# Kernel tuning notes

Hardware: AMD Instinct MI355X
Metric: run time of the kernel (lower is better)

## Reference

```python
import jax, jax.numpy as jnp
import numpy as np

N, L, D, H = 2, 2048, 1024, 16
DK = D // H  # 64


def setup_inputs() -> dict:
    key = jax.random.key(0)
    ks = jax.random.split(key, 8)
    Xq = jax.random.normal(ks[0], (N, L, D), dtype=jnp.float32)
    Xk = jax.random.normal(ks[1], (N, L, D), dtype=jnp.float32)
    Xv = jax.random.normal(ks[2], (N, L, D), dtype=jnp.float32)
    mask_2d = jax.random.randint(ks[3], (N, L, L), 0, 2, dtype=jnp.int32)
    scale = 0.02
    Wq = jax.random.normal(ks[4], (D, D), dtype=jnp.float32) * scale
    Wk = jax.random.normal(ks[5], (D, D), dtype=jnp.float32) * scale
    Wv = jax.random.normal(ks[6], (D, D), dtype=jnp.float32) * scale
    Wo = jax.random.normal(ks[7], (D, D), dtype=jnp.float32) * scale
    return {"Xq": Xq, "Xk": Xk, "Xv": Xv, "Wq": Wq, "Wk": Wk, "Wv": Wv, "Wo": Wo, "mask_2d": mask_2d}


def reference(Xq, Xk, Xv, Wq, Wk, Wv, Wo, mask_2d):
    # Projections (bias=False). Per-head slicing in the original == reshape to [N,L,H,DK].
    Q = (Xq @ Wq).reshape(N, L, H, DK)
    K = (Xk @ Wk).reshape(N, L, H, DK)
    V = (Xv @ Wv).reshape(N, L, H, DK)
    # Scaled dot-product scores: [N, H, L, L]
    scores = jnp.einsum("blhd,bmhd->bhlm", Q, K) / jnp.sqrt(jnp.asarray(DK, scores_dtype(Q)))
    # NOTE: original uses masked_fill(mask==0, 0) BEFORE softmax (zero-fill, not -inf).
    scores = jnp.where(mask_2d[:, None, :, :] == 0, jnp.zeros((), scores.dtype), scores)
    A = jax.nn.softmax(scores, axis=-1)
    O = jnp.einsum("bhlm,bmhd->blhd", A, V).reshape(N, L, D)
    return O @ Wo


def scores_dtype(Q):
    return Q.dtype
```

## Files before the change

kernel.cpp:

```cpp
#include <hip/hip_runtime.h>
#include <hip/hip_bf16.h>

#define NB 2
#define L_SEQ 2048
#define NH 16
#define DKH 64
#define DMODEL 1024
#define MROWS (NB * L_SEQ)
#define QSCALE 0.18033688f
#define DD (DMODEL * DMODEL)

typedef __attribute__((ext_vector_type(8))) short short8;
typedef __attribute__((ext_vector_type(4))) float f32x4;
typedef __attribute__((ext_vector_type(2))) int int2v;
typedef __attribute__((ext_vector_type(4))) int int4v;

static __device__ __forceinline__ unsigned short f2bf(float f) {
    unsigned u = __float_as_uint(f);
    u += 0x7fffu + ((u >> 16) & 1u);
    return (unsigned short)(u >> 16);
}

static __device__ __forceinline__ float fexp2(float x) {
#if __has_builtin(__builtin_amdgcn_exp2f)
    return __builtin_amdgcn_exp2f(x);
#else
    return __expf(x * 0.6931471806f);
#endif
}

static __device__ __forceinline__ unsigned pk_bf16(float a, float b) {
    __hip_bfloat162 h = __float22bfloat162_rn(make_float2(a, b));
    return *reinterpret_cast<unsigned*>(&h);
}

static __device__ __forceinline__ void gll16(const void* g, void* l) {
    __builtin_amdgcn_global_load_lds(
        (const __attribute__((address_space(1))) void*)g,
        (__attribute__((address_space(3))) void*)l, 16, 0, 0);
}

static __device__ __forceinline__ int2v pl32swap(int a, int b) {
#if __has_builtin(__builtin_amdgcn_permlane32_swap)
    return __builtin_amdgcn_permlane32_swap(a, b, false, false);
#else
    const int pa = __shfl_xor(a, 32);
    const int pb = __shfl_xor(b, 32);
    const bool lo = ((threadIdx.x & 63) < 32);
    int2v r;
    r.x = lo ? a : pb;
    r.y = lo ? pa : b;
    return r;
#endif
}

static __device__ __forceinline__ int2v pl16swap(int a, int b) {
#if __has_builtin(__builtin_amdgcn_permlane16_swap)
    return __builtin_amdgcn_permlane16_swap(a, b, false, false);
#else
    const int pa = __shfl_xor(a, 16);
    const int pb = __shfl_xor(b, 16);
    const bool ev = (((threadIdx.x >> 4) & 1) == 0);
    int2v r;
    r.x = ev ? a : pb;
    r.y = ev ? pa : b;
    return r;
#endif
}

static __device__ __forceinline__ int sbfe1(int word, int off) {
#if __has_builtin(__builtin_amdgcn_sbfe)
    return __builtin_amdgcn_sbfe(word, off, 1);
#else
    return (word << (31 - off)) >> 31;
#endif
}

__global__ __launch_bounds__(256)
void prep(const float* __restrict__ Xq, const float* __restrict__ Xk,
          const float* __restrict__ Xv, const float* __restrict__ w0,
          const float* __restrict__ w1, const float* __restrict__ w2,
          const float* __restrict__ w3, const int* __restrict__ mask,
          unsigned short* __restrict__ XB, unsigned short* __restrict__ WtB,
          unsigned long long* __restrict__ MWT)
{
    __shared__ float ts[32][33];
    const int bx = blockIdx.x;
    const int t  = threadIdx.x;

    if (bx < 12288) {
        const int z = bx >> 12;
        const float* src = (z == 0) ? Xq : (z == 1) ? Xk : Xv;
        const size_t i4 = (size_t)(bx & 4095) * 256 + t;
        float4 v = ((const float4*)src)[i4];
        ushort4 o;
        o.x = f2bf(v.x); o.y = f2bf(v.y); o.z = f2bf(v.z); o.w = f2bf(v.w);
        ((ushort4*)(XB + (size_t)z * 4194304))[i4] = o;
    } else if (bx < 16384) {
        const int idx = bx - 12288;
        const int z   = idx >> 10;
        const int rem = idx & 1023;
        const float* W = (z == 0) ? w0 : (z == 1) ? w1 : (z == 2) ? w2 : w3;
        unsigned short* Wt = WtB + (size_t)z * DD;
        const int n0 = (rem & 31) * 32;
        const int k0 = (rem >> 5) * 32;
        const int r  = t >> 3;
        const int c  = (t & 7) * 4;
        float4 v = *(const float4*)&W[(size_t)(k0 + r) * DMODEL + n0 + c];
        ts[r][c + 0] = v.x; ts[r][c + 1] = v.y;
        ts[r][c + 2] = v.z; ts[r][c + 3] = v.w;
        __syncthreads();
        ushort4 o;
        o.x = f2bf(ts[c + 0][r]); o.y = f2bf(ts[c + 1][r]);
        o.z = f2bf(ts[c + 2][r]); o.w = f2bf(ts[c + 3][r]);
        *(ushort4*)&Wt[(size_t)(n0 + r) * DMODEL + k0 + c] = o;
    } else {
        const int lane = t & 63;
        const size_t wbase = (size_t)(bx - 16384) * 4 + (t >> 6);
#pragma unroll
        for (int it = 0; it < 8; ++it) {
            const size_t wid = wbase + (size_t)it * 16384;
            const int mv = mask[wid * 64 + lane];
            const unsigned long long bits = __ballot(mv != 0);
            if (lane == 0) {
                const int b   = (int)(wid >> 16);
                const int rem = (int)(wid & 65535);
                const int row = rem >> 5;
                const int wd  = rem & 31;
                MWT[((size_t)b * 32 + wd) * L_SEQ + row] = bits;
            }
        }
    }
}

__global__ __launch_bounds__(256)
void gemm_qkv(const unsigned short* __restrict__ XB,
              const unsigned short* __restrict__ WtB,
              unsigned short* __restrict__ QKV)
{
    __shared__ __align__(16) unsigned short SMEM[16384];

    const int t    = threadIdx.x;
    const int w    = t >> 6;
    const int lane = t & 63;

    const int bid   = blockIdx.x;
    const int xcd   = bid & 7;
    const int idx   = bid >> 3;
    const int pair  = xcd * 12 + (idx >> 3);
    const int n0    = (idx & 7) * 128;
    const int m0    = (pair & 31) * 128;
    const int z     = pair >> 5;

    const unsigned short* A = XB  + (size_t)z * ((size_t)MROWS * DMODEL);
    const unsigned short* B = WtB + (size_t)z * DD;

    const int srow = lane >> 2;
    const int sc4  = (lane & 3) ^ (srow & 3);

    const unsigned short* ag[2];
    const unsigned short* bg[2];
    int lao[2], lbo[2];
#pragma unroll
    for (int g = 0; g < 2; ++g) {
        const int R = w * 32 + g * 16;
        ag[g] = A + (size_t)(m0 + R + srow) * DMODEL + sc4 * 8;
        bg[g] = B + (size_t)(n0 + R + srow) * DMODEL + sc4 * 8;
        lao[g] = R * 32;
        lbo[g] = R * 32;
    }

    const int ml = lane & 15;
    const int q  = lane >> 4;
    const int wm = (w >> 1) * 64;
    const int wn = (w & 1) * 64;

    const f32x4 z4 = {0.f, 0.f, 0.f, 0.f};
    f32x4 acc[4][4];
#pragma unroll
    for (int i = 0; i < 4; ++i)
#pragma unroll
        for (int j = 0; j < 4; ++j) acc[i][j] = z4;

#pragma unroll
    for (int g = 0; g < 2; ++g) {
        gll16(ag[g], &SMEM[lao[g]]);
        gll16(bg[g], &SMEM[8192 + lbo[g]]);
    }

    for (int j = 0; j < 32; ++j) {
        const int cur = j & 1;
        __syncthreads();
        if (j < 31) {
            const int kt = (j + 1) * 32;
            const int nb = (cur ^ 1) * 4096;
#pragma unroll
            for (int g = 0; g < 2; ++g) {
                gll16(ag[g] + kt, &SMEM[nb + lao[g]]);
                gll16(bg[g] + kt, &SMEM[8192 + nb + lbo[g]]);
            }
        }
        const unsigned short* As = &SMEM[cur * 4096];
        const unsigned short* Bs = &SMEM[8192 + cur * 4096];
        short8 av[4], bv[4];
#pragma unroll
        for (int mt = 0; mt < 4; ++mt)
            av[mt] = *(const short8*)
                &As[(wm + mt * 16 + ml) * 32 + ((q ^ (ml & 3)) * 8)];
#pragma unroll
        for (int nt = 0; nt < 4; ++nt)
            bv[nt] = *(const short8*)
                &Bs[(wn + nt * 16 + ml) * 32 + ((q ^ (ml & 3)) * 8)];
#pragma unroll
        for (int mt = 0; mt < 4; ++mt)
#pragma unroll
            for (int nt = 0; nt < 4; ++nt)
                acc[mt][nt] = __builtin_amdgcn_mfma_f32_16x16x32_bf16(
                    av[mt], bv[nt], acc[mt][nt], 0, 0, 0);
    }

    unsigned short* O = QKV + (size_t)z * ((size_t)MROWS * DMODEL);
    __syncthreads();
    unsigned short* Ts = SMEM;

    if (z == 2) {
#pragma unroll
        for (int mt = 0; mt < 4; ++mt) {
            const int trow0 = wm + mt * 16 + q * 4;
            const int ch    = trow0 >> 3;
#pragma unroll
            for (int nt = 0; nt < 4; ++nt) {
                const int tcol = wn + nt * 16 + ml;
                const int pc   = (ch & 8) | ((ch & 7) ^ (tcol & 7));
                ushort4 pv;
                pv.x = f2bf(acc[mt][nt][0]); pv.y = f2bf(acc[mt][nt][1]);
                pv.z = f2bf(acc[mt][nt][2]); pv.w = f2bf(acc[mt][nt][3]);
                *(ushort4*)&Ts[tcol * 128 + pc * 8 + (trow0 & 7)] = pv;
            }
        }
        __syncthreads();
        const int bb = m0 >> 11;
        const int l0 = (m0 & (L_SEQ - 1)) + (t & 15) * 8;
        const int cr = t & 15;
#pragma unroll
        for (int it = 0; it < 8; ++it) {
            const int tcol = (t >> 4) + 16 * it;
            const int pc   = (cr & 8) | ((cr & 7) ^ (tcol & 7));
            short8 vv = *(const short8*)&Ts[tcol * 128 + pc * 8];
            const int n  = n0 + tcol;
            const int hh = n >> 6;
            const int dk = n & (DKH - 1);
            *(short8*)&O[((size_t)(bb * NH + hh) * DKH + dk) * L_SEQ + l0] = vv;
        }
    } else {
        const float qs = (z == 0) ? QSCALE : 1.0f;
#pragma unroll
        for (int mt = 0; mt < 4; ++mt) {
            const int row0 = wm + mt * 16 + q * 4;
#pragma unroll
            for (int nt = 0; nt < 4; ++nt) {
                const int col = wn + nt * 16 + ml;
#pragma unroll
                for (int r = 0; r < 4; ++r)
                    Ts[(row0 + r) * 128 + col] = f2bf(acc[mt][nt][r] * qs);
            }
        }
        __syncthreads();
        const int mloc = t >> 3;
        const int c0   = t & 7;
#pragma unroll
        for (int pass = 0; pass < 4; ++pass) {
#pragma unroll
            for (int half = 0; half < 2; ++half) {
                const int m = mloc + 32 * pass;
                const int c = c0 + 8 * half;
                short8 v = *(const short8*)&Ts[m * 128 + c * 8];
                const int row = m0 + m;
                const int bb  = row >> 11;
                const int l   = row & (L_SEQ - 1);
                const int n   = n0 + c * 8;
                const int hh  = n >> 6;
                const int dk  = n & (DKH - 1);
                *(short8*)&O[(((size_t)(bb * NH + hh) * L_SEQ + l) << 6) + dk] = v;
            }
        }
    }
}

__global__ __launch_bounds__(256)
void gemm_out(const unsigned short* __restrict__ OB,
              const unsigned short* __restrict__ Wt,
              float* __restrict__ out)
{
    __shared__ __align__(16) unsigned short As[2][2048];
    __shared__ __align__(16) unsigned short Bs[2][4096];

    const int t    = threadIdx.x;
    const int w    = t >> 6;
    const int lane = t & 63;

    const int bid = blockIdx.x;
    const int xcd = bid & 7;
    const int idx = bid >> 3;
    const int n0  = (idx & 7) * 128;
    const int m0  = (xcd * 8 + (idx >> 3)) * 64;

    const int srow = lane >> 2;
    const int sc4  = (lane & 3) ^ (srow & 3);

    const unsigned short* ag =
        OB + (size_t)(m0 + w * 16 + srow) * DMODEL + sc4 * 8;
    const unsigned short* bg[2];
    int lbo[2];
#pragma unroll
    for (int g = 0; g < 2; ++g) {
        const int R = w * 32 + g * 16;
        bg[g] = Wt + (size_t)(n0 + R + srow) * DMODEL + sc4 * 8;
        lbo[g] = R * 32;
    }
    const int lao = (w * 16) * 32;

    const int ml = lane & 15;
    const int q  = lane >> 4;
    const int wm = (w >> 1) * 32;
    const int wn = (w & 1) * 64;

    const f32x4 z4 = {0.f, 0.f, 0.f, 0.f};
    f32x4 acc[2][4];
#pragma unroll
    for (int i = 0; i < 2; ++i)
#pragma unroll
        for (int j = 0; j < 4; ++j) acc[i][j] = z4;

    gll16(ag, &As[0][lao]);
#pragma unroll
    for (int g = 0; g < 2; ++g) gll16(bg[g], &Bs[0][lbo[g]]);

    for (int j = 0; j < 32; ++j) {
        const int cur = j & 1;
        __syncthreads();
        if (j < 31) {
            const int kt = (j + 1) * 32;
            gll16(ag + kt, &As[cur ^ 1][lao]);
#pragma unroll
            for (int g = 0; g < 2; ++g)
                gll16(bg[g] + kt, &Bs[cur ^ 1][lbo[g]]);
        }
        short8 av[2], bv[4];
#pragma unroll
        for (int mt = 0; mt < 2; ++mt)
            av[mt] = *(const short8*)
                &As[cur][(wm + mt * 16 + ml) * 32 + ((q ^ (ml & 3)) * 8)];
#pragma unroll
        for (int nt = 0; nt < 4; ++nt)
            bv[nt] = *(const short8*)
                &Bs[cur][(wn + nt * 16 + ml) * 32 + ((q ^ (ml & 3)) * 8)];
#pragma unroll
        for (int mt = 0; mt < 2; ++mt)
#pragma unroll
            for (int nt = 0; nt < 4; ++nt)
                acc[mt][nt] = __builtin_amdgcn_mfma_f32_16x16x32_bf16(
                    av[mt], bv[nt], acc[mt][nt], 0, 0, 0);
    }

#pragma unroll
    for (int mt = 0; mt < 2; ++mt) {
        const int gr0 = m0 + wm + mt * 16 + q * 4;
#pragma unroll
        for (int nt = 0; nt < 4; ++nt) {
            const int col = n0 + wn + nt * 16 + ml;
#pragma unroll
            for (int r = 0; r < 4; ++r)
                out[(size_t)(gr0 + r) * DMODEL + col] = acc[mt][nt][r];
        }
    }
}

__global__ __launch_bounds__(512, 4)
void attn_mfma(const unsigned short* __restrict__ Qb,
               const unsigned short* __restrict__ Kb,
               const unsigned short* __restrict__ Vtb,
               const unsigned long long* __restrict__ MWT,
               unsigned short* __restrict__ OB)
{
    __shared__ __align__(16) unsigned short Ks[2][64 * 64];
    __shared__ __align__(16) unsigned short Vts[2][64 * 64];
    __shared__ __align__(16) unsigned long long MskL[2][128];

    const int t    = threadIdx.x;
    const int w    = t >> 6;
    const int lane = t & 63;
    const int ml   = lane & 15;
    const int quad = lane >> 4;

    const int bid = blockIdx.x;
    const int xcd = bid & 7;
    const int idx = bid >> 3;
    const int p   = xcd * 4 + (idx >> 4);
    const int jq  = idx & 15;
    const int h   = p & 15;
    const int b   = p >> 4;
    const int q0  = jq * 128;

    const size_t hoff = (size_t)(b * NH + h) * L_SEQ * DKH;
    const unsigned short* Qh  = Qb  + hoff;
    const unsigned short* Kh  = Kb  + hoff;
    const unsigned short* Vth = Vtb + hoff;

    const int srow = lane >> 3;
    const int sc   = (lane & 7) ^ srow;

    unsigned short* QL = &Ks[0][0];
    gll16(Qh + (size_t)(q0 + w * 16 + srow) * DKH + sc * 8,
          &QL[(w * 16) * 64]);
    gll16(Qh + (size_t)(q0 + w * 16 + 8 + srow) * DKH + sc * 8,
          &QL[(w * 16 + 8) * 64]);

    const unsigned short* kg = Kh + (size_t)(w * 8 + srow) * DKH + sc * 8;
    const unsigned short* vg = Vth + (size_t)(w * 8 + srow) * L_SEQ + sc * 8;

    short8 kr = *(const short8*)kg;  kg += 64 * DKH;
    short8 vr = *(const short8*)vg;  vg += 64;

    const unsigned long long* mg = MWT + (size_t)b * 32 * L_SEQ + q0 + t;
    unsigned long long m_pf = 0;
    if (t < 128) m_pf = mg[0];

    __syncthreads();

    short8 qf[2];
#pragma unroll
    for (int s = 0; s < 2; ++s)
        qf[s] = *(const short8*)
            &QL[(w * 16 + ml) * 64 + (((s * 4 + quad) ^ (ml & 7)) * 8)];

    __syncthreads();

    *(short8*)&Ks[0][(w * 8) * 64 + lane * 8]  = kr;
    *(short8*)&Vts[0][(w * 8) * 64 + lane * 8] = vr;
    if (t < 128) MskL[0][t] = m_pf;

    kr = *(const short8*)kg;  kg += 64 * DKH;
    vr = *(const short8*)vg;  vg += 64;
    if (t < 128) m_pf = mg[L_SEQ];

    f32x4 oacc[4];
    const f32x4 z4 = {0.f, 0.f, 0.f, 0.f};
#pragma unroll
    for (int dt = 0; dt < 4; ++dt) oacc[dt] = z4;
    float l_i = 0.f;

    __syncthreads();

    for (int j = 0; j < 32; ++j) {
        const int cur = j & 1;
        if (j < 31) {
            const int nxt = cur ^ 1;
            *(short8*)&Ks[nxt][(w * 8) * 64 + lane * 8]  = kr;
            *(short8*)&Vts[nxt][(w * 8) * 64 + lane * 8] = vr;
            if (t < 128) MskL[nxt][t] = m_pf;
            if (j < 30) {
                kr = *(const short8*)kg;  kg += 64 * DKH;
                vr = *(const short8*)vg;  vg += 64;
                if (t < 128) m_pf = mg[(size_t)(j + 2) * L_SEQ];
            }
        }

        f32x4 sacc[4];
#pragma unroll
        for (int kt = 0; kt < 4; ++kt) sacc[kt] = z4;
#pragma unroll
        for (int s = 0; s < 2; ++s) {
            short8 kf[4];
#pragma unroll
            for (int kt = 0; kt < 4; ++kt)
                kf[kt] = *(const short8*)
                    &Ks[cur][(kt * 16 + ml) * 64 +
                             (((s * 4 + quad) ^ (ml & 7)) * 8)];
#pragma unroll
            for (int kt = 0; kt < 4; ++kt)
                sacc[kt] = __builtin_amdgcn_mfma_f32_16x16x32_bf16(
                    kf[kt], qf[s], sacc[kt], 0, 0, 0);
        }

        const unsigned long long wq = MskL[cur][w * 16 + ml] >> (quad * 4);
        const unsigned mlo = (unsigned)wq;
        const unsigned mhi = (unsigned)(wq >> 32);
        float rs = 0.f;
        float pr[4][4];
#pragma unroll
        for (int kt = 0; kt < 4; ++kt) {
            const int word = (int)((kt < 2) ? mlo : mhi);
            const int base = (kt & 1) * 16;
#pragma unroll
            for (int r = 0; r < 4; ++r) {
                const int mm = sbfe1(word, base + r);
                const float sm =
                    __int_as_float(__float_as_int(sacc[kt][r]) & mm);
                const float e = fexp2(sm);
                pr[kt][r] = e;
                rs += e;
            }
        }
        rs += __shfl_xor(rs, 16);
        rs += __shfl_xor(rs, 32);
        l_i += rs;

        int p01[4], p23[4];
#pragma unroll
        for (int kt = 0; kt < 4; ++kt) {
            p01[kt] = (int)pk_bf16(pr[kt][0], pr[kt][1]);
            p23[kt] = (int)pk_bf16(pr[kt][2], pr[kt][3]);
        }

#pragma unroll
        for (int s = 0; s < 2; ++s) {
            const int2v w01 = pl32swap(p01[2 * s], p01[2 * s + 1]);
            const int2v r01 = pl16swap(w01.x, w01.y);
            const int2v w23 = pl32swap(p23[2 * s], p23[2 * s + 1]);
            const int2v r23 = pl16swap(w23.x, w23.y);
            int4v pw;
            pw.x = r01.x; pw.y = r23.x; pw.z = r01.y; pw.w = r23.y;
            const short8 pf = __builtin_bit_cast(short8, pw);
#pragma unroll
            for (int dt = 0; dt < 4; ++dt) {
                const short8 vf = *(const short8*)
                    &Vts[cur][(dt * 16 + ml) * 64 +
                              (((s * 4 + quad) ^ (ml & 7)) * 8)];
                oacc[dt] = __builtin_amdgcn_mfma_f32_16x16x32_bf16(
                    vf, pf, oacc[dt], 0, 0, 0);
            }
        }

        __syncthreads();
    }

    const float inv = 1.0f / l_i;
    const int qrow = q0 + w * 16 + ml;
#pragma unroll
    for (int dt = 0; dt < 4; ++dt) {
        ushort4 o4;
        o4.x = f2bf(oacc[dt][0] * inv);
        o4.y = f2bf(oacc[dt][1] * inv);
        o4.z = f2bf(oacc[dt][2] * inv);
        o4.w = f2bf(oacc[dt][3] * inv);
        *(ushort4*)&OB[(size_t)(b * L_SEQ + qrow) * DMODEL + h * DKH +
                       dt * 16 + quad * 4] = o4;
    }
}

extern "C" void kernel_launch(void* const* d_in, const int* in_sizes, int n_in,
                              void* d_out, int out_size, void* d_ws, size_t ws_size,
                              hipStream_t stream)
{
    (void)in_sizes; (void)n_in; (void)out_size; (void)ws_size;

    const float* Xq   = (const float*)d_in[0];
    const float* Xk   = (const float*)d_in[1];
    const float* Xv   = (const float*)d_in[2];
    const float* Wq   = (const float*)d_in[3];
    const float* Wk   = (const float*)d_in[4];
    const float* Wv   = (const float*)d_in[5];
    const float* Wo   = (const float*)d_in[6];
    const int*   mask = (const int*)d_in[7];
    float* out = (float*)d_out;

    char* base = (char*)d_ws;
    unsigned short*     XB  = (unsigned short*)base;
    unsigned short*     WtB = (unsigned short*)(base + (24u << 20));
    unsigned short*     QKV = (unsigned short*)(base + (32u << 20));
    unsigned short*     OB  = (unsigned short*)(base + (56u << 20));
    unsigned long long* MWT = (unsigned long long*)(base + (64u << 20));

    const size_t tsz = (size_t)MROWS * DMODEL;

    prep<<<dim3(20480), 256, 0, stream>>>(
        Xq, Xk, Xv, Wq, Wk, Wv, Wo, mask, XB, WtB, MWT);

    gemm_qkv<<<dim3(768), 256, 0, stream>>>(XB, WtB, QKV);

    attn_mfma<<<dim3(512), 512, 0, stream>>>(
        QKV, QKV + tsz, QKV + 2 * tsz, MWT, OB);

    gemm_out<<<dim3(512), 256, 0, stream>>>(OB, WtB + 3 * (size_t)DD, out);
}
```

Baseline: 251.9 us.

## Split attention KV tile across wave groups with 2x2 query/key register tiling

The 8 waves are regrouped into 4 query slices of 32 rows and 2 key halves, so each wave processes two 16-row query tiles against half of each 64-key block. Each K/V LDS fragment is reused across two MFMAs, which halves per-wave LDS reads. The two key-half groups reduce their partial outputs and row sums through shared memory at the end. K/V staging also switches from register round-trips to direct global-to-LDS loads (gll16). In exchange the kernel carries more accumulator registers and adds an epilogue reduction with one more barrier.

```diff
diff --git a/kernel.cpp b/kernel.cpp
--- a/kernel.cpp
+++ b/kernel.cpp
@@ -383,8 +383,7 @@
                const unsigned long long* __restrict__ MWT,
                unsigned short* __restrict__ OB)
 {
-    __shared__ __align__(16) unsigned short Ks[2][64 * 64];
-    __shared__ __align__(16) unsigned short Vts[2][64 * 64];
+    __shared__ __align__(16) unsigned short SH[16384];
     __shared__ __align__(16) unsigned long long MskL[2][128];
 
     const int t    = threadIdx.x;
@@ -392,6 +391,8 @@
     const int lane = t & 63;
     const int ml   = lane & 15;
     const int quad = lane >> 4;
+    const int qs   = w & 3;
+    const int g    = w >> 2;
 
     const int bid = blockIdx.x;
     const int xcd = bid & 7;
@@ -410,142 +411,171 @@
     const int srow = lane >> 3;
     const int sc   = (lane & 7) ^ srow;
 
-    unsigned short* QL = &Ks[0][0];
     gll16(Qh + (size_t)(q0 + w * 16 + srow) * DKH + sc * 8,
-          &QL[(w * 16) * 64]);
+          &SH[(w * 16) * 64]);
     gll16(Qh + (size_t)(q0 + w * 16 + 8 + srow) * DKH + sc * 8,
-          &QL[(w * 16 + 8) * 64]);
-
-    const unsigned short* kg = Kh + (size_t)(w * 8 + srow) * DKH + sc * 8;
-    const unsigned short* vg = Vth + (size_t)(w * 8 + srow) * L_SEQ + sc * 8;
-
-    short8 kr = *(const short8*)kg;  kg += 64 * DKH;
-    short8 vr = *(const short8*)vg;  vg += 64;
-
-    const unsigned long long* mg = MWT + (size_t)b * 32 * L_SEQ + q0 + t;
+          &SH[(w * 16 + 8) * 64]);
+
+    const unsigned long long* mg =
+        MWT + (size_t)b * 32 * L_SEQ + q0 + (t & 127);
     unsigned long long m_pf = 0;
     if (t < 128) m_pf = mg[0];
 
     __syncthreads();
 
-    short8 qf[2];
-#pragma unroll
-    for (int s = 0; s < 2; ++s)
-        qf[s] = *(const short8*)
-            &QL[(w * 16 + ml) * 64 + (((s * 4 + quad) ^ (ml & 7)) * 8)];
+    short8 qf[2][2];
+#pragma unroll
+    for (int qn = 0; qn < 2; ++qn)
+#pragma unroll
+        for (int s = 0; s < 2; ++s)
+            qf[qn][s] = *(const short8*)
+                &SH[(qs * 32 + qn * 16 + ml) * 64 +
+                    (((s * 4 + quad) ^ (ml & 7)) * 8)];
 
     __syncthreads();
 
-    *(short8*)&Ks[0][(w * 8) * 64 + lane * 8]  = kr;
-    *(short8*)&Vts[0][(w * 8) * 64 + lane * 8] = vr;
-    if (t < 128) MskL[0][t] = m_pf;
-
-    kr = *(const short8*)kg;  kg += 64 * DKH;
-    vr = *(const short8*)vg;  vg += 64;
-    if (t < 128) m_pf = mg[L_SEQ];
-
-    f32x4 oacc[4];
+    gll16(Kh + (size_t)(w * 8 + srow) * DKH + sc * 8, &SH[(w * 8) * 64]);
+    gll16(Vth + (size_t)(w * 8 + srow) * L_SEQ + sc * 8,
+          &SH[8192 + (w * 8) * 64]);
+    if (t < 128) { MskL[0][t] = m_pf; m_pf = mg[L_SEQ]; }
+
+    const unsigned short* kg = Kh + (size_t)(64 + w * 8 + srow) * DKH + sc * 8;
+    const unsigned short* vg = Vth + (size_t)(w * 8 + srow) * L_SEQ + 64 + sc * 8;
+
+    f32x4 oacc[2][4];
     const f32x4 z4 = {0.f, 0.f, 0.f, 0.f};
 #pragma unroll
-    for (int dt = 0; dt < 4; ++dt) oacc[dt] = z4;
-    float l_i = 0.f;
+    for (int qn = 0; qn < 2; ++qn)
+#pragma unroll
+        for (int dt = 0; dt < 4; ++dt) oacc[qn][dt] = z4;
+    float l_i[2] = {0.f, 0.f};
 
     __syncthreads();
 
     for (int j = 0; j < 32; ++j) {
         const int cur = j & 1;
         if (j < 31) {
-            const int nxt = cur ^ 1;
-            *(short8*)&Ks[nxt][(w * 8) * 64 + lane * 8]  = kr;
-            *(short8*)&Vts[nxt][(w * 8) * 64 + lane * 8] = vr;
-            if (t < 128) MskL[nxt][t] = m_pf;
-            if (j < 30) {
-                kr = *(const short8*)kg;  kg += 64 * DKH;
-                vr = *(const short8*)vg;  vg += 64;
-                if (t < 128) m_pf = mg[(size_t)(j + 2) * L_SEQ];
-            }
-        }
-
-        f32x4 sacc[4];
-#pragma unroll
-        for (int kt = 0; kt < 4; ++kt) sacc[kt] = z4;
+            const int nb = (cur ^ 1) * 4096;
+            gll16(kg, &SH[nb + (w * 8) * 64]);           kg += 64 * DKH;
+            gll16(vg, &SH[8192 + nb + (w * 8) * 64]);    vg += 64;
+            if (t < 128) {
+                MskL[cur ^ 1][t] = m_pf;
+                if (j < 30) m_pf = mg[(size_t)(j + 2) * L_SEQ];
+            }
+        }
+
+        const unsigned short* Kc = &SH[cur * 4096];
+        const unsigned short* Vc = &SH[8192 + cur * 4096];
+
+        f32x4 sacc[2][2];
+#pragma unroll
+        for (int qn = 0; qn < 2; ++qn)
+#pragma unroll
+            for (int kt = 0; kt < 2; ++kt) sacc[qn][kt] = z4;
 #pragma unroll
         for (int s = 0; s < 2; ++s) {
-            short8 kf[4];
-#pragma unroll
-            for (int kt = 0; kt < 4; ++kt)
-                kf[kt] = *(const short8*)
-                    &Ks[cur][(kt * 16 + ml) * 64 +
-                             (((s * 4 + quad) ^ (ml & 7)) * 8)];
-#pragma unroll
-            for (int kt = 0; kt < 4; ++kt)
-                sacc[kt] = __builtin_amdgcn_mfma_f32_16x16x32_bf16(
-                    kf[kt], qf[s], sacc[kt], 0, 0, 0);
-        }
-
-        const unsigned long long wq = MskL[cur][w * 16 + ml] >> (quad * 4);
-        const unsigned mlo = (unsigned)wq;
-        const unsigned mhi = (unsigned)(wq >> 32);
-        float rs = 0.f;
-        float pr[4][4];
-#pragma unroll
-        for (int kt = 0; kt < 4; ++kt) {
-            const int word = (int)((kt < 2) ? mlo : mhi);
-            const int base = (kt & 1) * 16;
-#pragma unroll
-            for (int r = 0; r < 4; ++r) {
-                const int mm = sbfe1(word, base + r);
-                const float sm =
-                    __int_as_float(__float_as_int(sacc[kt][r]) & mm);
-                const float e = fexp2(sm);
-                pr[kt][r] = e;
-                rs += e;
-            }
-        }
-        rs += __shfl_xor(rs, 16);
-        rs += __shfl_xor(rs, 32);
-        l_i += rs;
-
-        int p01[4], p23[4];
-#pragma unroll
-        for (int kt = 0; kt < 4; ++kt) {
-            p01[kt] = (int)pk_bf16(pr[kt][0], pr[kt][1]);
-            p23[kt] = (int)pk_bf16(pr[kt][2], pr[kt][3]);
-        }
-
-#pragma unroll
-        for (int s = 0; s < 2; ++s) {
-            const int2v w01 = pl32swap(p01[2 * s], p01[2 * s + 1]);
+            const int swz = ((s * 4 + quad) ^ (ml & 7)) * 8;
+            const short8 kf0 = *(const short8*)&Kc[(g * 32 + ml) * 64 + swz];
+            const short8 kf1 = *(const short8*)&Kc[(g * 32 + 16 + ml) * 64 + swz];
+#pragma unroll
+            for (int qn = 0; qn < 2; ++qn) {
+                sacc[qn][0] = __builtin_amdgcn_mfma_f32_16x16x32_bf16(
+                    kf0, qf[qn][s], sacc[qn][0], 0, 0, 0);
+                sacc[qn][1] = __builtin_amdgcn_mfma_f32_16x16x32_bf16(
+                    kf1, qf[qn][s], sacc[qn][1], 0, 0, 0);
+            }
+        }
+
+        short8 pf[2];
+#pragma unroll
+        for (int qn = 0; qn < 2; ++qn) {
+            const unsigned long long wqf = MskL[cur][qs * 32 + qn * 16 + ml];
+            const int word = (int)(unsigned)(wqf >> (g * 32 + quad * 4));
+            float rs = 0.f;
+            float pr[2][4];
+#pragma unroll
+            for (int kt = 0; kt < 2; ++kt) {
+#pragma unroll
+                for (int r = 0; r < 4; ++r) {
+                    const int mm = sbfe1(word, kt * 16 + r);
+                    const float sm =
+                        __int_as_float(__float_as_int(sacc[qn][kt][r]) & mm);
+                    const float e = fexp2(sm);
+                    pr[kt][r] = e;
+                    rs += e;
+                }
+            }
+            rs += __shfl_xor(rs, 16);
+            rs += __shfl_xor(rs, 32);
+            l_i[qn] += rs;
+
+            int p01[2], p23[2];
+#pragma unroll
+            for (int kt = 0; kt < 2; ++kt) {
+                p01[kt] = (int)pk_bf16(pr[kt][0], pr[kt][1]);
+                p23[kt] = (int)pk_bf16(pr[kt][2], pr[kt][3]);
+            }
+            const int2v w01 = pl32swap(p01[0], p01[1]);
             const int2v r01 = pl16swap(w01.x, w01.y);
-            const int2v w23 = pl32swap(p23[2 * s], p23[2 * s + 1]);
+            const int2v w23 = pl32swap(p23[0], p23[1]);
             const int2v r23 = pl16swap(w23.x, w23.y);
             int4v pw;
             pw.x = r01.x; pw.y = r23.x; pw.z = r01.y; pw.w = r23.y;
-            const short8 pf = __builtin_bit_cast(short8, pw);
+            pf[qn] = __builtin_bit_cast(short8, pw);
+        }
+
+        {
+            const int swz = ((g * 4 + quad) ^ (ml & 7)) * 8;
 #pragma unroll
             for (int dt = 0; dt < 4; ++dt) {
                 const short8 vf = *(const short8*)
-                    &Vts[cur][(dt * 16 + ml) * 64 +
-                              (((s * 4 + quad) ^ (ml & 7)) * 8)];
-                oacc[dt] = __builtin_amdgcn_mfma_f32_16x16x32_bf16(
-                    vf, pf, oacc[dt], 0, 0, 0);
+                    &Vc[(dt * 16 + ml) * 64 + swz];
+#pragma unroll
+                for (int qn = 0; qn < 2; ++qn)
+                    oacc[qn][dt] = __builtin_amdgcn_mfma_f32_16x16x32_bf16(
+                        vf, pf[qn], oacc[qn][dt], 0, 0, 0);
             }
         }
 
         __syncthreads();
     }
 
-    const float inv = 1.0f / l_i;
-    const int qrow = q0 + w * 16 + ml;
-#pragma unroll
-    for (int dt = 0; dt < 4; ++dt) {
-        ushort4 o4;
-        o4.x = f2bf(oacc[dt][0] * inv);
-        o4.y = f2bf(oacc[dt][1] * inv);
-        o4.z = f2bf(oacc[dt][2] * inv);
-        o4.w = f2bf(oacc[dt][3] * inv);
-        *(ushort4*)&OB[(size_t)(b * L_SEQ + qrow) * DMODEL + h * DKH +
-                       dt * 16 + quad * 4] = o4;
+    float* OP = (float*)SH;
+    float* LP = (float*)&MskL[0][0];
+    const int basel = qs * 64 + lane;
+    if (g == 1) {
+#pragma unroll
+        for (int qn = 0; qn < 2; ++qn) {
+#pragma unroll
+            for (int dt = 0; dt < 4; ++dt)
+#pragma unroll
+                for (int r = 0; r < 4; ++r)
+                    OP[(qn * 16 + dt * 4 + r) * 256 + basel] = oacc[qn][dt][r];
+            LP[qn * 256 + basel] = l_i[qn];
+        }
+    }
+    __syncthreads();
+    if (g == 0) {
+#pragma unroll
+        for (int qn = 0; qn < 2; ++qn) {
+            const float l = l_i[qn] + LP[qn * 256 + basel];
+            const float inv = 1.0f / l;
+            const int qrow = q0 + qs * 32 + qn * 16 + ml;
+#pragma unroll
+            for (int dt = 0; dt < 4; ++dt) {
+                ushort4 o4;
+                o4.x = f2bf((oacc[qn][dt][0] +
+                             OP[(qn * 16 + dt * 4 + 0) * 256 + basel]) * inv);
+                o4.y = f2bf((oacc[qn][dt][1] +
+                             OP[(qn * 16 + dt * 4 + 1) * 256 + basel]) * inv);
+                o4.z = f2bf((oacc[qn][dt][2] +
+                             OP[(qn * 16 + dt * 4 + 2) * 256 + basel]) * inv);
+                o4.w = f2bf((oacc[qn][dt][3] +
+                             OP[(qn * 16 + dt * 4 + 3) * 256 + basel]) * inv);
+                *(ushort4*)&OB[(size_t)(b * L_SEQ + qrow) * DMODEL + h * DKH +
+                               dt * 16 + quad * 4] = o4;
+            }
+        }
     }
 }
 
```

After: 250.9 us. Within noise of the previous version (-0.4%).

## Fuse fp32-to-bf16 input conversion into QKV GEMM and add MFMA setprio

Applied to the files above, without the earlier changes.

Removes the separate pass that converted Xq/Xk/Xv to bf16 in the prep kernel. The QKV GEMM now loads fp32 A tiles into registers, packs them to bf16 and stores them to LDS after the MFMA work, which overlaps with compute. This drops a 24MB write and re-read of the converted inputs. In exchange the GEMM reads fp32 A, which is twice the bytes, and the A tile now goes through registers instead of direct global-to-LDS loads. The attention kernel also wraps its MFMA sections in s_setprio to raise wave priority during matrix work.

```diff
diff --git a/kernel.cpp b/kernel.cpp
--- a/kernel.cpp
+++ b/kernel.cpp
@@ -77,27 +77,17 @@
 }
 
 __global__ __launch_bounds__(256)
-void prep(const float* __restrict__ Xq, const float* __restrict__ Xk,
-          const float* __restrict__ Xv, const float* __restrict__ w0,
-          const float* __restrict__ w1, const float* __restrict__ w2,
-          const float* __restrict__ w3, const int* __restrict__ mask,
-          unsigned short* __restrict__ XB, unsigned short* __restrict__ WtB,
-          unsigned long long* __restrict__ MWT)
+void prep(const float* __restrict__ w0, const float* __restrict__ w1,
+          const float* __restrict__ w2, const float* __restrict__ w3,
+          const int* __restrict__ mask,
+          unsigned short* __restrict__ WtB, unsigned long long* __restrict__ MWT)
 {
     __shared__ float ts[32][33];
     const int bx = blockIdx.x;
     const int t  = threadIdx.x;
 
-    if (bx < 12288) {
-        const int z = bx >> 12;
-        const float* src = (z == 0) ? Xq : (z == 1) ? Xk : Xv;
-        const size_t i4 = (size_t)(bx & 4095) * 256 + t;
-        float4 v = ((const float4*)src)[i4];
-        ushort4 o;
-        o.x = f2bf(v.x); o.y = f2bf(v.y); o.z = f2bf(v.z); o.w = f2bf(v.w);
-        ((ushort4*)(XB + (size_t)z * 4194304))[i4] = o;
-    } else if (bx < 16384) {
-        const int idx = bx - 12288;
+    if (bx < 4096) {
+        const int idx = bx;
         const int z   = idx >> 10;
         const int rem = idx & 1023;
         const float* W = (z == 0) ? w0 : (z == 1) ? w1 : (z == 2) ? w2 : w3;
@@ -116,7 +106,7 @@
         *(ushort4*)&Wt[(size_t)(n0 + r) * DMODEL + k0 + c] = o;
     } else {
         const int lane = t & 63;
-        const size_t wbase = (size_t)(bx - 16384) * 4 + (t >> 6);
+        const size_t wbase = (size_t)(bx - 4096) * 4 + (t >> 6);
 #pragma unroll
         for (int it = 0; it < 8; ++it) {
             const size_t wid = wbase + (size_t)it * 16384;
@@ -134,7 +124,8 @@
 }
 
 __global__ __launch_bounds__(256)
-void gemm_qkv(const unsigned short* __restrict__ XB,
+void gemm_qkv(const float* __restrict__ Xq, const float* __restrict__ Xk,
+              const float* __restrict__ Xv,
               const unsigned short* __restrict__ WtB,
               unsigned short* __restrict__ QKV)
 {
@@ -152,19 +143,19 @@
     const int m0    = (pair & 31) * 128;
     const int z     = pair >> 5;
 
-    const unsigned short* A = XB  + (size_t)z * ((size_t)MROWS * DMODEL);
+    const float* Af = (z == 0) ? Xq : (z == 1) ? Xk : Xv;
     const unsigned short* B = WtB + (size_t)z * DD;
 
     const int srow = lane >> 2;
     const int sc4  = (lane & 3) ^ (srow & 3);
 
-    const unsigned short* ag[2];
+    const float* agf[2];
     const unsigned short* bg[2];
     int lao[2], lbo[2];
 #pragma unroll
     for (int g = 0; g < 2; ++g) {
         const int R = w * 32 + g * 16;
-        ag[g] = A + (size_t)(m0 + R + srow) * DMODEL + sc4 * 8;
+        agf[g] = Af + (size_t)(m0 + R + srow) * DMODEL + sc4 * 8;
         bg[g] = B + (size_t)(n0 + R + srow) * DMODEL + sc4 * 8;
         lao[g] = R * 32;
         lbo[g] = R * 32;
@@ -182,21 +173,33 @@
 #pragma unroll
         for (int j = 0; j < 4; ++j) acc[i][j] = z4;
 
+    float4 a0[2], a1[2];
 #pragma unroll
     for (int g = 0; g < 2; ++g) {
-        gll16(ag[g], &SMEM[lao[g]]);
+        a0[g] = *(const float4*)agf[g];
+        a1[g] = *(const float4*)(agf[g] + 4);
         gll16(bg[g], &SMEM[8192 + lbo[g]]);
+    }
+#pragma unroll
+    for (int g = 0; g < 2; ++g) {
+        int4v pw;
+        pw.x = (int)pk_bf16(a0[g].x, a0[g].y);
+        pw.y = (int)pk_bf16(a0[g].z, a0[g].w);
+        pw.z = (int)pk_bf16(a1[g].x, a1[g].y);
+        pw.w = (int)pk_bf16(a1[g].z, a1[g].w);
+        *(int4v*)&SMEM[lao[g] + lane * 8] = pw;
     }
 
     for (int j = 0; j < 32; ++j) {
         const int cur = j & 1;
         __syncthreads();
+        const int nb = (cur ^ 1) * 4096;
         if (j < 31) {
             const int kt = (j + 1) * 32;
-            const int nb = (cur ^ 1) * 4096;
 #pragma unroll
             for (int g = 0; g < 2; ++g) {
-                gll16(ag[g] + kt, &SMEM[nb + lao[g]]);
+                a0[g] = *(const float4*)(agf[g] + kt);
+                a1[g] = *(const float4*)(agf[g] + kt + 4);
                 gll16(bg[g] + kt, &SMEM[8192 + nb + lbo[g]]);
             }
         }
@@ -217,6 +220,17 @@
             for (int nt = 0; nt < 4; ++nt)
                 acc[mt][nt] = __builtin_amdgcn_mfma_f32_16x16x32_bf16(
                     av[mt], bv[nt], acc[mt][nt], 0, 0, 0);
+        if (j < 31) {
+#pragma unroll
+            for (int g = 0; g < 2; ++g) {
+                int4v pw;
+                pw.x = (int)pk_bf16(a0[g].x, a0[g].y);
+                pw.y = (int)pk_bf16(a0[g].z, a0[g].w);
+                pw.z = (int)pk_bf16(a1[g].x, a1[g].y);
+                pw.w = (int)pk_bf16(a1[g].z, a1[g].w);
+                *(int4v*)&SMEM[nb + lao[g] + lane * 8] = pw;
+            }
+        }
     }
 
     unsigned short* O = QKV + (size_t)z * ((size_t)MROWS * DMODEL);
@@ -469,6 +483,7 @@
         f32x4 sacc[4];
 #pragma unroll
         for (int kt = 0; kt < 4; ++kt) sacc[kt] = z4;
+        __builtin_amdgcn_s_setprio(1);
 #pragma unroll
         for (int s = 0; s < 2; ++s) {
             short8 kf[4];
@@ -482,6 +497,7 @@
                 sacc[kt] = __builtin_amdgcn_mfma_f32_16x16x32_bf16(
                     kf[kt], qf[s], sacc[kt], 0, 0, 0);
         }
+        __builtin_amdgcn_s_setprio(0);
 
         const unsigned long long wq = MskL[cur][w * 16 + ml] >> (quad * 4);
         const unsigned mlo = (unsigned)wq;
@@ -522,6 +538,7 @@
             int4v pw;
             pw.x = r01.x; pw.y = r23.x; pw.z = r01.y; pw.w = r23.y;
             const short8 pf = __builtin_bit_cast(short8, pw);
+            __builtin_amdgcn_s_setprio(1);
 #pragma unroll
             for (int dt = 0; dt < 4; ++dt) {
                 const short8 vf = *(const short8*)
@@ -530,6 +547,7 @@
                 oacc[dt] = __builtin_amdgcn_mfma_f32_16x16x32_bf16(
                     vf, pf, oacc[dt], 0, 0, 0);
             }
+            __builtin_amdgcn_s_setprio(0);
         }
 
         __syncthreads();
@@ -566,7 +584,6 @@
     float* out = (float*)d_out;
 
     char* base = (char*)d_ws;
-    unsigned short*     XB  = (unsigned short*)base;
     unsigned short*     WtB = (unsigned short*)(base + (24u << 20));
     unsigned short*     QKV = (unsigned short*)(base + (32u << 20));
     unsigned short*     OB  = (unsigned short*)(base + (56u << 20));
@@ -574,10 +591,10 @@
 
     const size_t tsz = (size_t)MROWS * DMODEL;
 
-    prep<<<dim3(20480), 256, 0, stream>>>(
-        Xq, Xk, Xv, Wq, Wk, Wv, Wo, mask, XB, WtB, MWT);
-
-    gemm_qkv<<<dim3(768), 256, 0, stream>>>(XB, WtB, QKV);
+    prep<<<dim3(8192), 256, 0, stream>>>(
+        Wq, Wk, Wv, Wo, mask, WtB, MWT);
+
+    gemm_qkv<<<dim3(768), 256, 0, stream>>>(Xq, Xk, Xv, WtB, QKV);
 
     attn_mfma<<<dim3(512), 512, 0, stream>>>(
         QKV, QKV + tsz, QKV + 2 * tsz, MWT, OB);
```

Result: slower. 269.5 us (+7.0%).

## Split key dimension across wave groups in attention, doubling block count

Applied to the files above, without the earlier changes.

Each attention block now handles 64 query rows instead of 128. The 8 waves form two groups, and each group processes half of every 64-key tile for its 16 query rows. The two partial output accumulators and row sums are combined through shared memory at the end. This doubles the grid to 1024 blocks for more parallelism and occupancy, and halves per-wave score work. The cost is that every K/V tile is loaded by twice as many blocks, plus an extra reduction and barrier at the end.

```diff
diff --git a/kernel.cpp b/kernel.cpp
--- a/kernel.cpp
+++ b/kernel.cpp
@@ -385,22 +385,24 @@
 {
     __shared__ __align__(16) unsigned short Ks[2][64 * 64];
     __shared__ __align__(16) unsigned short Vts[2][64 * 64];
-    __shared__ __align__(16) unsigned long long MskL[2][128];
+    __shared__ __align__(16) unsigned long long MskL[2][64];
 
     const int t    = threadIdx.x;
     const int w    = t >> 6;
     const int lane = t & 63;
     const int ml   = lane & 15;
     const int quad = lane >> 4;
+    const int qs   = w & 3;
+    const int g    = w >> 2;
 
     const int bid = blockIdx.x;
     const int xcd = bid & 7;
     const int idx = bid >> 3;
-    const int p   = xcd * 4 + (idx >> 4);
-    const int jq  = idx & 15;
+    const int p   = xcd * 4 + (idx >> 5);
+    const int jq  = idx & 31;
     const int h   = p & 15;
     const int b   = p >> 4;
-    const int q0  = jq * 128;
+    const int q0  = jq * 64;
 
     const size_t hoff = (size_t)(b * NH + h) * L_SEQ * DKH;
     const unsigned short* Qh  = Qb  + hoff;
@@ -411,10 +413,7 @@
     const int sc   = (lane & 7) ^ srow;
 
     unsigned short* QL = &Ks[0][0];
-    gll16(Qh + (size_t)(q0 + w * 16 + srow) * DKH + sc * 8,
-          &QL[(w * 16) * 64]);
-    gll16(Qh + (size_t)(q0 + w * 16 + 8 + srow) * DKH + sc * 8,
-          &QL[(w * 16 + 8) * 64]);
+    gll16(Qh + (size_t)(q0 + w * 8 + srow) * DKH + sc * 8, &QL[(w * 8) * 64]);
 
     const unsigned short* kg = Kh + (size_t)(w * 8 + srow) * DKH + sc * 8;
     const unsigned short* vg = Vth + (size_t)(w * 8 + srow) * L_SEQ + sc * 8;
@@ -424,7 +423,7 @@
 
     const unsigned long long* mg = MWT + (size_t)b * 32 * L_SEQ + q0 + t;
     unsigned long long m_pf = 0;
-    if (t < 128) m_pf = mg[0];
+    if (t < 64) m_pf = mg[0];
 
     __syncthreads();
 
@@ -432,17 +431,17 @@
 #pragma unroll
     for (int s = 0; s < 2; ++s)
         qf[s] = *(const short8*)
-            &QL[(w * 16 + ml) * 64 + (((s * 4 + quad) ^ (ml & 7)) * 8)];
+            &QL[(qs * 16 + ml) * 64 + (((s * 4 + quad) ^ (ml & 7)) * 8)];
 
     __syncthreads();
 
     *(short8*)&Ks[0][(w * 8) * 64 + lane * 8]  = kr;
     *(short8*)&Vts[0][(w * 8) * 64 + lane * 8] = vr;
-    if (t < 128) MskL[0][t] = m_pf;
+    if (t < 64) MskL[0][t] = m_pf;
 
     kr = *(const short8*)kg;  kg += 64 * DKH;
     vr = *(const short8*)vg;  vg += 64;
-    if (t < 128) m_pf = mg[L_SEQ];
+    if (t < 64) m_pf = mg[L_SEQ];
 
     f32x4 oacc[4];
     const f32x4 z4 = {0.f, 0.f, 0.f, 0.f};
@@ -458,43 +457,38 @@
             const int nxt = cur ^ 1;
             *(short8*)&Ks[nxt][(w * 8) * 64 + lane * 8]  = kr;
             *(short8*)&Vts[nxt][(w * 8) * 64 + lane * 8] = vr;
-            if (t < 128) MskL[nxt][t] = m_pf;
+            if (t < 64) MskL[nxt][t] = m_pf;
             if (j < 30) {
                 kr = *(const short8*)kg;  kg += 64 * DKH;
                 vr = *(const short8*)vg;  vg += 64;
-                if (t < 128) m_pf = mg[(size_t)(j + 2) * L_SEQ];
-            }
-        }
-
-        f32x4 sacc[4];
-#pragma unroll
-        for (int kt = 0; kt < 4; ++kt) sacc[kt] = z4;
+                if (t < 64) m_pf = mg[(size_t)(j + 2) * L_SEQ];
+            }
+        }
+
+        f32x4 sacc[2];
+        sacc[0] = z4; sacc[1] = z4;
 #pragma unroll
         for (int s = 0; s < 2; ++s) {
-            short8 kf[4];
-#pragma unroll
-            for (int kt = 0; kt < 4; ++kt)
-                kf[kt] = *(const short8*)
-                    &Ks[cur][(kt * 16 + ml) * 64 +
-                             (((s * 4 + quad) ^ (ml & 7)) * 8)];
-#pragma unroll
-            for (int kt = 0; kt < 4; ++kt)
-                sacc[kt] = __builtin_amdgcn_mfma_f32_16x16x32_bf16(
-                    kf[kt], qf[s], sacc[kt], 0, 0, 0);
-        }
-
-        const unsigned long long wq = MskL[cur][w * 16 + ml] >> (quad * 4);
-        const unsigned mlo = (unsigned)wq;
-        const unsigned mhi = (unsigned)(wq >> 32);
+            const int swz = ((s * 4 + quad) ^ (ml & 7)) * 8;
+            const short8 kf0 = *(const short8*)
+                &Ks[cur][(g * 32 + ml) * 64 + swz];
+            const short8 kf1 = *(const short8*)
+                &Ks[cur][(g * 32 + 16 + ml) * 64 + swz];
+            sacc[0] = __builtin_amdgcn_mfma_f32_16x16x32_bf16(
+                kf0, qf[s], sacc[0], 0, 0, 0);
+            sacc[1] = __builtin_amdgcn_mfma_f32_16x16x32_bf16(
+                kf1, qf[s], sacc[1], 0, 0, 0);
+        }
+
+        const unsigned long long wqf = MskL[cur][qs * 16 + ml];
+        const int word = (int)(unsigned)(wqf >> (g * 32 + quad * 4));
         float rs = 0.f;
-        float pr[4][4];
-#pragma unroll
-        for (int kt = 0; kt < 4; ++kt) {
-            const int word = (int)((kt < 2) ? mlo : mhi);
-            const int base = (kt & 1) * 16;
+        float pr[2][4];
+#pragma unroll
+        for (int kt = 0; kt < 2; ++kt) {
 #pragma unroll
             for (int r = 0; r < 4; ++r) {
-                const int mm = sbfe1(word, base + r);
+                const int mm = sbfe1(word, kt * 16 + r);
                 const float sm =
                     __int_as_float(__float_as_int(sacc[kt][r]) & mm);
                 const float e = fexp2(sm);
@@ -506,27 +500,26 @@
         rs += __shfl_xor(rs, 32);
         l_i += rs;
 
-        int p01[4], p23[4];
-#pragma unroll
-        for (int kt = 0; kt < 4; ++kt) {
+        int p01[2], p23[2];
+#pragma unroll
+        for (int kt = 0; kt < 2; ++kt) {
             p01[kt] = (int)pk_bf16(pr[kt][0], pr[kt][1]);
             p23[kt] = (int)pk_bf16(pr[kt][2], pr[kt][3]);
         }
-
-#pragma unroll
-        for (int s = 0; s < 2; ++s) {
-            const int2v w01 = pl32swap(p01[2 * s], p01[2 * s + 1]);
-            const int2v r01 = pl16swap(w01.x, w01.y);
-            const int2v w23 = pl32swap(p23[2 * s], p23[2 * s + 1]);
-            const int2v r23 = pl16swap(w23.x, w23.y);
-            int4v pw;
-            pw.x = r01.x; pw.y = r23.x; pw.z = r01.y; pw.w = r23.y;
-            const short8 pf = __builtin_bit_cast(short8, pw);
+        const int2v w01 = pl32swap(p01[0], p01[1]);
+        const int2v r01 = pl16swap(w01.x, w01.y);
+        const int2v w23 = pl32swap(p23[0], p23[1]);
+        const int2v r23 = pl16swap(w23.x, w23.y);
+        int4v pw;
+        pw.x = r01.x; pw.y = r23.x; pw.z = r01.y; pw.w = r23.y;
+        const short8 pf = __builtin_bit_cast(short8, pw);
+
+        {
+            const int swz = ((g * 4 + quad) ^ (ml & 7)) * 8;
 #pragma unroll
             for (int dt = 0; dt < 4; ++dt) {
                 const short8 vf = *(const short8*)
-                    &Vts[cur][(dt * 16 + ml) * 64 +
-                              (((s * 4 + quad) ^ (ml & 7)) * 8)];
+                    &Vts[cur][(dt * 16 + ml) * 64 + swz];
                 oacc[dt] = __builtin_amdgcn_mfma_f32_16x16x32_bf16(
                     vf, pf, oacc[dt], 0, 0, 0);
             }
@@ -535,17 +528,32 @@
         __syncthreads();
     }
 
-    const float inv = 1.0f / l_i;
-    const int qrow = q0 + w * 16 + ml;
-#pragma unroll
-    for (int dt = 0; dt < 4; ++dt) {
-        ushort4 o4;
-        o4.x = f2bf(oacc[dt][0] * inv);
-        o4.y = f2bf(oacc[dt][1] * inv);
-        o4.z = f2bf(oacc[dt][2] * inv);
-        o4.w = f2bf(oacc[dt][3] * inv);
-        *(ushort4*)&OB[(size_t)(b * L_SEQ + qrow) * DMODEL + h * DKH +
-                       dt * 16 + quad * 4] = o4;
+    float* OP = (float*)&Ks[0][0];
+    float* LP = (float*)&MskL[0][0];
+    const int basel = qs * 64 + lane;
+    if (g == 1) {
+#pragma unroll
+        for (int dt = 0; dt < 4; ++dt)
+#pragma unroll
+            for (int r = 0; r < 4; ++r)
+                OP[(dt * 4 + r) * 256 + basel] = oacc[dt][r];
+        LP[basel] = l_i;
+    }
+    __syncthreads();
+    if (g == 0) {
+        const float l = l_i + LP[basel];
+        const float inv = 1.0f / l;
+        const int qrow = q0 + qs * 16 + ml;
+#pragma unroll
+        for (int dt = 0; dt < 4; ++dt) {
+            ushort4 o4;
+            o4.x = f2bf((oacc[dt][0] + OP[(dt * 4 + 0) * 256 + basel]) * inv);
+            o4.y = f2bf((oacc[dt][1] + OP[(dt * 4 + 1) * 256 + basel]) * inv);
+            o4.z = f2bf((oacc[dt][2] + OP[(dt * 4 + 2) * 256 + basel]) * inv);
+            o4.w = f2bf((oacc[dt][3] + OP[(dt * 4 + 3) * 256 + basel]) * inv);
+            *(ushort4*)&OB[(size_t)(b * L_SEQ + qrow) * DMODEL + h * DKH +
+                           dt * 16 + quad * 4] = o4;
+        }
     }
 }
 
@@ -579,7 +587,7 @@
 
     gemm_qkv<<<dim3(768), 256, 0, stream>>>(XB, WtB, QKV);
 
-    attn_mfma<<<dim3(512), 512, 0, stream>>>(
+    attn_mfma<<<dim3(1024), 512, 0, stream>>>(
         QKV, QKV + tsz, QKV + 2 * tsz, MWT, OB);
 
     gemm_out<<<dim3(512), 256, 0, stream>>>(OB, WtB + 3 * (size_t)DD, out);
```

Measured after the change: 253.3 us. Within noise of the previous version (+0.5%).
